# Kernel optimization log

Measured on AMD Instinct MI355X. Metric: run time of the kernel, lower is better.

Reference implementation:

```python
import jax, jax.numpy as jnp
from jax import lax
import numpy as np

B, L, D, H, SH = 4, 1024, 512, 8, 256
MLP_H = 4 * D
GAMMA, BETA = 0.1, 1.0
SIG_A, SIG_B = 1.0, 0.5
BIG = 1e9


def setup_inputs() -> dict:
    key = jax.random.key(0)
    ks = jax.random.split(key, 8)

    def lin(k, fin, fout):
        return jax.random.normal(k, (fin, fout), jnp.float32) * (1.0 / np.sqrt(fin))

    inp = {}
    inp["x"] = jax.random.normal(ks[0], (B, L, D), jnp.float32)
    inp["ln1_g"] = jnp.ones((D,), jnp.float32)
    inp["ln1_b"] = jnp.zeros((D,), jnp.float32)
    inp["ln2_g"] = jnp.ones((D,), jnp.float32)
    inp["ln2_b"] = jnp.zeros((D,), jnp.float32)
    inp["qkv_w"] = lin(ks[1], D, 3 * D)
    inp["qkv_b"] = jnp.zeros((3 * D,), jnp.float32)
    inp["proj_w"] = lin(ks[2], D, D)
    inp["proj_b"] = jnp.zeros((D,), jnp.float32)
    inp["fc1_w"] = lin(ks[3], D, MLP_H)
    inp["fc1_b"] = jnp.zeros((MLP_H,), jnp.float32)
    inp["fc2_w"] = lin(ks[4], MLP_H, D)
    inp["fc2_b"] = jnp.zeros((D,), jnp.float32)
    # 4 SigmaNets (norm1, attn, norm2, mlp) stacked on leading axis
    inp["sig_w1"] = jax.random.normal(ks[5], (4, D, SH), jnp.float32) * (1.0 / np.sqrt(D))
    inp["sig_b1"] = jnp.zeros((4, SH), jnp.float32)
    inp["sig_w2"] = jax.random.normal(ks[6], (4, SH, D), jnp.float32) * (1.0 / np.sqrt(SH))
    inp["sig_b2"] = jnp.zeros((4, D), jnp.float32)
    return inp


def layernorm(x, g, b, eps=1e-5):
    m = x.mean(-1, keepdims=True)
    v = ((x - m) ** 2).mean(-1, keepdims=True)
    return (x - m) / jnp.sqrt(v + eps) * g + b


def sigmanet(x, w1, b1, w2, b2):
    # (B,L,D) -> (B,L,1), sigma = a*sigmoid(mean(fc2(relu(fc1(x))))) + b
    h = jax.nn.relu(x @ w1 + b1)
    o = h @ w2 + b2
    m = o.mean(-1, keepdims=True)
    return SIG_A * jax.nn.sigmoid(m) + SIG_B


def attention(x, qkv_w, qkv_b, proj_w, proj_b):
    b_, l_, d_ = x.shape
    hd = d_ // H
    qkv = (x @ qkv_w + qkv_b).reshape(b_, l_, 3, H, hd)
    q, k, v = qkv[:, :, 0], qkv[:, :, 1], qkv[:, :, 2]  # (B,L,H,hd)
    scores = jnp.einsum("bqhd,bkhd->bhqk", q, k) * (hd ** -0.5)
    attn = jax.nn.softmax(scores, axis=-1)
    out = jnp.einsum("bhqk,bkhd->bqhd", attn, v).reshape(b_, l_, d_)
    return out @ proj_w + proj_b


def mlp(x, fc1_w, fc1_b, fc2_w, fc2_b):
    return jax.nn.gelu(x @ fc1_w + fc1_b, approximate=False) @ fc2_w + fc2_b


def soft_dtw(C, gamma):
    # soft-min DP over (B, N, N) cost matrix via anti-diagonal scan
    b_, n_, m_ = C.shape
    i_arr = jnp.arange(n_)

    def step(carry, k):
        d2, d1 = carry  # diagonals k-2, k-1; entry i holds R[i, (k-?)-i]
        j = k - i_arr
        valid = (j >= 0) & (j < m_)
        jc = jnp.clip(j, 0, m_ - 1)
        Cd = jnp.where(valid[None, :], C[:, i_arr, jc], BIG)
        pad = jnp.full((b_, 1), BIG, C.dtype)
        a = jnp.concatenate([pad, d2[:, :-1]], axis=1)  # R[i-1, j-1]
        a = a.at[:, 0].set(jnp.where(k == 0, 0.0, a[:, 0]))  # virtual R[-1,-1]=0
        bdiag = jnp.concatenate([pad, d1[:, :-1]], axis=1)  # R[i-1, j]
        c = d1  # R[i, j-1]
        smin = -gamma * jax.nn.logsumexp(-jnp.stack([a, bdiag, c], 0) / gamma, axis=0)
        new = jnp.where(valid[None, :], Cd + smin, BIG)
        return (d1, new), None

    init = (jnp.full((b_, n_), BIG, C.dtype), jnp.full((b_, n_), BIG, C.dtype))
    (_, last), _ = lax.scan(step, init, jnp.arange(n_ + m_ - 1))
    return last[:, n_ - 1]  # R[N-1, M-1]


def udtw(x, y, sx, sy):
    # pairwise squared distances without (B,L,L,D) intermediate
    x2 = jnp.sum(x * x, -1)  # (B,L)
    y2 = jnp.sum(y * y, -1)
    Dm = x2[:, :, None] + y2[:, None, :] - 2.0 * jnp.einsum("bnd,bmd->bnm", x, y)
    Dm = jnp.maximum(Dm, 0.0)
    Sig = sx ** 2 + jnp.swapaxes(sy, 1, 2) ** 2  # (B,L,L) sigma_i^2 + sigma_j^2
    d = soft_dtw(Dm / Sig, GAMMA)               # uncertainty-weighted distance path
    s = soft_dtw(BETA * jnp.log(Sig), GAMMA)    # sigma regularization path
    return d, s


def reference(x, ln1_g, ln1_b, ln2_g, ln2_b, qkv_w, qkv_b, proj_w, proj_b,
              fc1_w, fc1_b, fc2_w, fc2_b, sig_w1, sig_b1, sig_w2, sig_b2):
    orig = x
    attn_out = attention(layernorm(x, ln1_g, ln1_b), qkv_w, qkv_b, proj_w, proj_b)
    sigma_x = sigmanet(orig, sig_w1[0], sig_b1[0], sig_w2[0], sig_b2[0])
    sigma_attn = sigmanet(attn_out, sig_w1[1], sig_b1[1], sig_w2[1], sig_b2[1])
    d_a, s_a = udtw(orig, attn_out, sigma_x, sigma_attn)
    x = x + attn_out * sigma_attn  # merge_mode == 'mul'
    mlp_out = mlp(layernorm(x, ln2_g, ln2_b), fc1_w, fc1_b, fc2_w, fc2_b)
    sigma_x2 = sigmanet(orig, sig_w1[2], sig_b1[2], sig_w2[2], sig_b2[2])
    sigma_mlp = sigmanet(mlp_out, sig_w1[3], sig_b1[3], sig_w2[3], sig_b2[3])
    d_m, s_m = udtw(orig, mlp_out, sigma_x2, sigma_mlp)
    l_ = x.shape[1]
    aux_loss = (d_a.mean() + s_a.mean() + d_m.mean() + s_m.mean()) / (l_ * l_)
    x = x + mlp_out * sigma_mlp
    return x, aux_loss
```

## Files before the change

### kernel.cpp

```cpp
#include <hip/hip_runtime.h>
#include <math.h>

typedef unsigned short ushort;
typedef __attribute__((ext_vector_type(8))) short short8;
typedef __attribute__((ext_vector_type(4))) short short4v;
typedef __attribute__((ext_vector_type(4))) float f32x4;

#define DEVI static __device__ __forceinline__

constexpr int Bq = 4, Lq = 1024, Dq = 512, Hq = 8, SHq = 256;
constexpr int Mrows = Bq * Lq;
constexpr float BIGF = 1e9f;
constexpr int PSTR = 1048576 + 16;

DEVI float bf2f(ushort u) { union { unsigned u; float f; } v; v.u = ((unsigned)u) << 16; return v.f; }
DEVI float bf2f(short s) { return bf2f((ushort)s); }
DEVI ushort f2bf(float f) {
  union { float f; unsigned u; } v; v.f = f;
  unsigned r = v.u + 0x7fffu + ((v.u >> 16) & 1u);
  return (ushort)(r >> 16);
}
DEVI float wave_sum(float x) { for (int o = 1; o < 64; o <<= 1) x += __shfl_xor(x, o, 64); return x; }
DEVI float readin(const void* p, long i, int isf32) {
  return isf32 ? ((const float*)p)[i] : bf2f(((const ushort*)p)[i]);
}

__global__ void detect_kern(const unsigned* __restrict__ g, int* __restrict__ flag) {
  if (threadIdx.x == 0) flag[0] = (g[0] == 0x3F800000u) ? 1 : 0;
}

__global__ __launch_bounds__(256) void convx_kern(const void* __restrict__ src, ushort* __restrict__ dst,
                                                  long n, const int* __restrict__ flag) {
  const int f = *flag;
  for (long i = blockIdx.x * 256L + threadIdx.x; i < n; i += (long)gridDim.x * 256)
    dst[i] = f ? f2bf(((const float*)src)[i]) : ((const ushort*)src)[i];
}

__global__ __launch_bounds__(256) void conv9_kern(const void* p0, const void* p1, const void* p2,
                                                  const void* p3, const void* p4, const void* p5,
                                                  const void* p6, const void* p7, const void* p8,
                                                  ushort* __restrict__ dst, const int* __restrict__ flag) {
  const int off[10] = {0, 512, 1024, 1536, 2048, 3584, 4096, 6144, 6656, 7680};
  const void* ps[9] = {p0, p1, p2, p3, p4, p5, p6, p7, p8};
  const int b = blockIdx.x;
  const void* s = ps[b];
  const int n = off[b + 1] - off[b];
  const int f = *flag;
  for (int i = threadIdx.x; i < n; i += 256)
    dst[off[b] + i] = f ? f2bf(((const float*)s)[i]) : ((const ushort*)s)[i];
}

__global__ __launch_bounds__(256) void transpose_bf(const void* __restrict__ src,
                                                    ushort* __restrict__ dst, int R, int C,
                                                    const int* __restrict__ flag) {
  __shared__ ushort t[64][65];
  const int f = *flag;
  const int tx = threadIdx.x & 63, tg = threadIdx.x >> 6;
  const long base = (long)blockIdx.z * R * C;
  const int r0 = blockIdx.y * 64, c0 = blockIdx.x * 64;
#pragma unroll
  for (int i = 0; i < 16; ++i) {
    int y = tg * 16 + i;
    float v = readin(src, base + (long)(r0 + y) * C + c0 + tx, f);
    t[y][tx] = f2bf(v);
  }
  __syncthreads();
#pragma unroll
  for (int i = 0; i < 16; ++i) {
    int y = tg * 16 + i;
    dst[base + (long)(c0 + y) * R + r0 + tx] = t[tx][y];
  }
}

__global__ void w2bar_kern(const void* __restrict__ w2, float* __restrict__ w2bar,
                           const int* __restrict__ flag) {
  const int k = blockIdx.x, s = blockIdx.y, lane = threadIdx.x;
  const int f = *flag;
  float t = 0.f;
#pragma unroll
  for (int i = 0; i < 8; ++i) t += readin(w2, ((long)s * SHq + k) * Dq + lane * 8 + i, f);
  t = wave_sum(t);
  if (lane == 0) w2bar[s * SHq + k] = t * (1.f / Dq);
}
__global__ void b2bar_kern(const void* __restrict__ b2, float* __restrict__ b2bar,
                           const int* __restrict__ flag) {
  const int s = blockIdx.x, lane = threadIdx.x;
  const int f = *flag;
  float t = 0.f;
#pragma unroll
  for (int i = 0; i < 8; ++i) t += readin(b2, (long)s * Dq + lane * 8 + i, f);
  t = wave_sum(t);
  if (lane == 0) b2bar[s] = t * (1.f / Dq);
}

__global__ __launch_bounds__(256) void ln_kern(const ushort* __restrict__ x, const ushort* __restrict__ g,
                                               const ushort* __restrict__ b, ushort* __restrict__ out) {
  const int row = blockIdx.x * 4 + (threadIdx.x >> 6);
  const int lane = threadIdx.x & 63;
  short8 v = *(const short8*)(x + (long)row * Dq + lane * 8);
  float f[8]; float s = 0.f, s2 = 0.f;
#pragma unroll
  for (int i = 0; i < 8; ++i) { f[i] = bf2f(v[i]); s += f[i]; s2 += f[i] * f[i]; }
  s = wave_sum(s); s2 = wave_sum(s2);
  float mean = s * (1.f / Dq);
  float var = s2 * (1.f / Dq) - mean * mean;
  float rstd = rsqrtf(var + 1e-5f);
  short8 gv = *(const short8*)(g + lane * 8);
  short8 bv = *(const short8*)(b + lane * 8);
  short8 o;
#pragma unroll
  for (int i = 0; i < 8; ++i) o[i] = (short)f2bf((f[i] - mean) * rstd * bf2f(gv[i]) + bf2f(bv[i]));
  *(short8*)(out + (long)row * Dq + lane * 8) = o;
}

template<int EPI>
__global__ __launch_bounds__(256) void gemm_kern(
    const ushort* __restrict__ A, int lda, long sA,
    const ushort* __restrict__ Bt, int ldb, long sB,
    const ushort* __restrict__ bias,
    void* __restrict__ Cout, int ldc, long sC, int K,
    const float* __restrict__ vx2, const float* __restrict__ vy2,
    const float* __restrict__ vsx, const float* __restrict__ vsy) {
  constexpr int LDT = 40;
  __shared__ alignas(16) short As[128 * LDT];
  __shared__ alignas(16) short Bs[128 * LDT];
  const int tid = threadIdx.x, lane = tid & 63, wid = tid >> 6;
  const int wr = wid >> 1, wc = wid & 1;
  const int m0 = blockIdx.y * 128, n0 = blockIdx.x * 128;
  const int bz = blockIdx.z;
  const ushort* Ab = A + (long)bz * sA;
  const ushort* Bb = Bt + (long)bz * sB;
  const int sr = tid >> 2, sc = (tid & 3) * 8;
  const int lr = lane & 15, lk = (lane >> 4) * 8;
  f32x4 acc[4][4];
#pragma unroll
  for (int i = 0; i < 4; ++i)
#pragma unroll
    for (int j = 0; j < 4; ++j) acc[i][j] = f32x4{0.f, 0.f, 0.f, 0.f};

  for (int k0 = 0; k0 < K; k0 += 32) {
    short8 a0 = *(const short8*)(Ab + (long)(m0 + sr) * lda + k0 + sc);
    short8 a1 = *(const short8*)(Ab + (long)(m0 + sr + 64) * lda + k0 + sc);
    short8 b0 = *(const short8*)(Bb + (long)(n0 + sr) * ldb + k0 + sc);
    short8 b1 = *(const short8*)(Bb + (long)(n0 + sr + 64) * ldb + k0 + sc);
    __syncthreads();
    *(short8*)&As[sr * LDT + sc] = a0;
    *(short8*)&As[(sr + 64) * LDT + sc] = a1;
    *(short8*)&Bs[sr * LDT + sc] = b0;
    *(short8*)&Bs[(sr + 64) * LDT + sc] = b1;
    __syncthreads();
    short8 af[4], bg[4];
#pragma unroll
    for (int m = 0; m < 4; ++m) af[m] = *(const short8*)&As[(wr * 64 + m * 16 + lr) * LDT + lk];
#pragma unroll
    for (int n = 0; n < 4; ++n) bg[n] = *(const short8*)&Bs[(wc * 64 + n * 16 + lr) * LDT + lk];
#pragma unroll
    for (int m = 0; m < 4; ++m)
#pragma unroll
      for (int n = 0; n < 4; ++n)
        acc[m][n] = __builtin_amdgcn_mfma_f32_16x16x32_bf16(af[m], bg[n], acc[m][n], 0, 0, 0);
  }
  const int lq = (lane >> 4) * 4;
#pragma unroll
  for (int n = 0; n < 4; ++n) {
    const int col = n0 + wc * 64 + n * 16 + lr;
    float bia = 0.f, y2v = 0.f, syv = 0.f;
    if (EPI <= 2) { if (bias) bia = bf2f(bias[col]); }
    if (EPI == 3) { y2v = vy2[(long)bz * Lq + col]; float t = vsy[(long)bz * Lq + col]; syv = t * t; }
#pragma unroll
    for (int m = 0; m < 4; ++m) {
      f32x4 v = acc[m][n];
      if (EPI <= 2) {
#pragma unroll
        for (int q = 0; q < 4; ++q) {
          const int row = m0 + wr * 64 + m * 16 + lq + q;
          float c = v[q] + bia;
          if (EPI == 1) c = fmaxf(c, 0.f);
          if (EPI == 2) c = 0.5f * c * (1.f + erff(c * 0.70710678118654752f));
          ((ushort*)Cout)[(long)bz * sC + (long)row * ldc + col] = f2bf(c);
        }
      } else {
        const int row0 = m0 + wr * 64 + m * 16 + lq;
        f32x4 o;
#pragma unroll
        for (int q = 0; q < 4; ++q) {
          float x2v = vx2[(long)bz * Lq + row0 + q];
          float sxv = vsx[(long)bz * Lq + row0 + q];
          float dm = fmaxf(x2v + y2v - 2.f * v[q], 0.f);
          o[q] = dm / (sxv * sxv + syv);
        }
        *(f32x4*)((float*)Cout + (long)bz * sC + (long)col * 1024 + row0) = o;
      }
    }
  }
}

__global__ __launch_bounds__(256) void attn_kern(const ushort* __restrict__ qkv, ushort* __restrict__ octx) {
  const int qt = blockIdx.x, h = blockIdx.y, b = blockIdx.z;
  const int tid = threadIdx.x, lane = tid & 63, wid = tid >> 6;
  const int lr = lane & 15, lkg = lane >> 4;
  __shared__ alignas(16) short Ks[64 * 72];
  __shared__ alignas(16) short Vt[64 * 72];
  __shared__ alignas(16) short Ps[64 * 72];
  const long qrow0 = (long)b * Lq + qt * 64;
  short8 qf[2];
  {
    const ushort* qp = qkv + (qrow0 + wid * 16 + lr) * 1536 + h * 64;
    qf[0] = *(const short8*)(qp + lkg * 8);
    qf[1] = *(const short8*)(qp + 32 + lkg * 8);
  }
  f32x4 accO[4];
#pragma unroll
  for (int n = 0; n < 4; ++n) accO[n] = f32x4{0.f, 0.f, 0.f, 0.f};
  float mrun[4], lrun[4];
#pragma unroll
  for (int q = 0; q < 4; ++q) { mrun[q] = -1e30f; lrun[q] = 0.f; }

  for (int t = 0; t < 16; ++t) {
    __syncthreads();
#pragma unroll
    for (int i = 0; i < 2; ++i) {
      const int row = (tid >> 3) + i * 32;
      const int c8 = (tid & 7) * 8;
      const long gr = ((long)b * Lq + t * 64 + row) * 1536 + h * 64;
      short8 kv = *(const short8*)(qkv + gr + 512 + c8);
      *(short8*)&Ks[row * 72 + c8] = kv;
      short8 vv = *(const short8*)(qkv + gr + 1024 + c8);
#pragma unroll
      for (int j = 0; j < 8; ++j) Vt[(c8 + j) * 72 + row] = vv[j];
    }
    __syncthreads();
    f32x4 sf[4];
#pragma unroll
    for (int n = 0; n < 4; ++n) {
      sf[n] = f32x4{0.f, 0.f, 0.f, 0.f};
#pragma unroll
      for (int ks = 0; ks < 2; ++ks) {
        short8 bk = *(const short8*)&Ks[(n * 16 + lr) * 72 + ks * 32 + lkg * 8];
        sf[n] = __builtin_amdgcn_mfma_f32_16x16x32_bf16(qf[ks], bk, sf[n], 0, 0, 0);
      }
    }
#pragma unroll
    for (int n = 0; n < 4; ++n)
#pragma unroll
      for (int q = 0; q < 4; ++q) sf[n][q] *= 0.125f;
    float scl[4];
#pragma unroll
    for (int q = 0; q < 4; ++q) {
      float mx = fmaxf(fmaxf(sf[0][q], sf[1][q]), fmaxf(sf[2][q], sf[3][q]));
#pragma unroll
      for (int o = 1; o < 16; o <<= 1) mx = fmaxf(mx, __shfl_xor(mx, o, 64));
      float mnew = fmaxf(mrun[q], mx);
      scl[q] = __expf(mrun[q] - mnew);
      mrun[q] = mnew;
      float rs = 0.f;
#pragma unroll
      for (int n = 0; n < 4; ++n) { float pp = __expf(sf[n][q] - mnew); sf[n][q] = pp; rs += pp; }
#pragma unroll
      for (int o = 1; o < 16; o <<= 1) rs += __shfl_xor(rs, o, 64);
      lrun[q] = lrun[q] * scl[q] + rs;
    }
#pragma unroll
    for (int n = 0; n < 4; ++n)
#pragma unroll
      for (int q = 0; q < 4; ++q) accO[n][q] *= scl[q];
#pragma unroll
    for (int n = 0; n < 4; ++n)
#pragma unroll
      for (int q = 0; q < 4; ++q)
        Ps[(wid * 16 + lkg * 4 + q) * 72 + n * 16 + lr] = (short)f2bf(sf[n][q]);
    short8 pa[2];
    pa[0] = *(const short8*)&Ps[(wid * 16 + lr) * 72 + lkg * 8];
    pa[1] = *(const short8*)&Ps[(wid * 16 + lr) * 72 + 32 + lkg * 8];
#pragma unroll
    for (int n = 0; n < 4; ++n)
#pragma unroll
      for (int ks = 0; ks < 2; ++ks) {
        short8 bv = *(const short8*)&Vt[(n * 16 + lr) * 72 + ks * 32 + lkg * 8];
        accO[n] = __builtin_amdgcn_mfma_f32_16x16x32_bf16(pa[ks], bv, accO[n], 0, 0, 0);
      }
  }
#pragma unroll
  for (int n = 0; n < 4; ++n) {
    const int col = h * 64 + n * 16 + lr;
#pragma unroll
    for (int q = 0; q < 4; ++q) {
      const long row = qrow0 + wid * 16 + lkg * 4 + q;
      octx[row * 512 + col] = f2bf(accO[n][q] / fmaxf(lrun[q], 1e-30f));
    }
  }
}

__global__ __launch_bounds__(256) void rownorm2_kern(const ushort* __restrict__ x, float* __restrict__ out) {
  const int row = blockIdx.x * 4 + (threadIdx.x >> 6), lane = threadIdx.x & 63;
  short8 v = *(const short8*)(x + (long)row * Dq + lane * 8);
  float s = 0.f;
#pragma unroll
  for (int i = 0; i < 8; ++i) { float f = bf2f(v[i]); s += f * f; }
  s = wave_sum(s);
  if (lane == 0) out[row] = s;
}

__global__ __launch_bounds__(256) void sigma_reduce_kern(const ushort* __restrict__ h, const float* __restrict__ w2bar,
                                                         const float* __restrict__ b2bar, int set,
                                                         float* __restrict__ sigma) {
  const int row = blockIdx.x * 4 + (threadIdx.x >> 6), lane = threadIdx.x & 63;
  short4v hv = *(const short4v*)(h + (long)row * SHq + lane * 4);
  float s = 0.f;
#pragma unroll
  for (int i = 0; i < 4; ++i) s += bf2f(hv[i]) * w2bar[lane * 4 + i];
  s = wave_sum(s);
  if (lane == 0) {
    float m = s + b2bar[set];
    sigma[(long)set * Mrows + row] = 1.f / (1.f + __expf(-m)) + 0.5f;
  }
}

__global__ __launch_bounds__(256) void fuse1_kern(const ushort* __restrict__ x, const ushort* __restrict__ attn,
                                                  const float* __restrict__ sig, const ushort* __restrict__ g,
                                                  const ushort* __restrict__ bb, void* __restrict__ x1out,
                                                  ushort* __restrict__ xn2, const int* __restrict__ flag) {
  const int row = blockIdx.x * 4 + (threadIdx.x >> 6), lane = threadIdx.x & 63;
  const int isf32 = *flag;
  const float sg = sig[row];
  short8 xv = *(const short8*)(x + (long)row * Dq + lane * 8);
  short8 av = *(const short8*)(attn + (long)row * Dq + lane * 8);
  float f[8]; float s = 0.f, s2 = 0.f;
#pragma unroll
  for (int i = 0; i < 8; ++i) {
    f[i] = bf2f(xv[i]) + bf2f(av[i]) * sg;
    s += f[i]; s2 += f[i] * f[i];
  }
  if (isf32) {
    float* o32 = (float*)x1out + (long)row * Dq + lane * 8;
    *(f32x4*)o32 = f32x4{f[0], f[1], f[2], f[3]};
    *(f32x4*)(o32 + 4) = f32x4{f[4], f[5], f[6], f[7]};
  } else {
    short8 xo;
#pragma unroll
    for (int i = 0; i < 8; ++i) xo[i] = (short)f2bf(f[i]);
    *(short8*)((ushort*)x1out + (long)row * Dq + lane * 8) = xo;
  }
  s = wave_sum(s); s2 = wave_sum(s2);
  float mean = s * (1.f / Dq);
  float var = s2 * (1.f / Dq) - mean * mean;
  float rstd = rsqrtf(var + 1e-5f);
  short8 gv = *(const short8*)(g + lane * 8);
  short8 bv = *(const short8*)(bb + lane * 8);
  short8 o;
#pragma unroll
  for (int i = 0; i < 8; ++i) o[i] = (short)f2bf((f[i] - mean) * rstd * bf2f(gv[i]) + bf2f(bv[i]));
  *(short8*)(xn2 + (long)row * Dq + lane * 8) = o;
}

__global__ __launch_bounds__(256) void fuse2_kern(const ushort* __restrict__ mlp,
                                                  const float* __restrict__ sig, void* __restrict__ out,
                                                  const int* __restrict__ flag) {
  const int row = blockIdx.x * 4 + (threadIdx.x >> 6), lane = threadIdx.x & 63;
  const int isf32 = *flag;
  const float sg = sig[row];
  short8 mv = *(const short8*)(mlp + (long)row * Dq + lane * 8);
  if (isf32) {
    float* o32 = (float*)out + (long)row * Dq + lane * 8;
    f32x4 a = *(const f32x4*)o32;
    f32x4 b = *(const f32x4*)(o32 + 4);
#pragma unroll
    for (int i = 0; i < 4; ++i) a[i] += bf2f(mv[i]) * sg;
#pragma unroll
    for (int i = 0; i < 4; ++i) b[i] += bf2f(mv[4 + i]) * sg;
    *(f32x4*)o32 = a;
    *(f32x4*)(o32 + 4) = b;
  } else {
    ushort* o16 = (ushort*)out + (long)row * Dq + lane * 8;
    short8 xv = *(const short8*)o16;
    short8 o;
#pragma unroll
    for (int i = 0; i < 8; ++i) o[i] = (short)f2bf(bf2f(xv[i]) + bf2f(mv[i]) * sg);
    *(short8*)o16 = o;
  }
}

__global__ __launch_bounds__(128, 1) void dtw_kern(const float* __restrict__ Cta, const float* __restrict__ Ctm,
                                                   const float* __restrict__ sigma, float* __restrict__ res) {
  const int sid = blockIdx.x >> 2, b = blockIdx.x & 3;
  const int tid = threadIdx.x, lane = tid & 63, wid = tid >> 6;
  const bool isS = (sid & 1);
  __shared__ alignas(16) float smemf[18432];
  constexpr float LN2 = 0.69314718055994531f;

  float cur[16];
#pragma unroll
  for (int r = 0; r < 16; ++r) cur[r] = BIGF;
  float A = BIGF;
  float B = BIGF;
  float D = (lane == 0) ? 0.f : BIGF;

  if (!isS) {
    const float* Ct = ((sid == 0) ? Cta : Ctm) + (long)b * PSTR;

#define PRODUCE2(S0)                                                           \
    {                                                                          \
      f32x4 L[4][8];                                                           \
      _Pragma("unroll")                                                        \
      for (int j = 0; j < 4; ++j) {                                            \
        const int ss = (S0) + j;                                               \
        int cA = 2 * ss - 2 * lane;                                            \
        int cB = cA + 1;                                                       \
        cA = cA < 0 ? 0 : (cA > 1023 ? 1023 : cA);                             \
        cB = cB < 0 ? 0 : (cB > 1023 ? 1023 : cB);                             \
        const float* gA = Ct + (long)cA * 1024 + lane * 16;                    \
        const float* gB = Ct + (long)cB * 1024 + lane * 16;                    \
        _Pragma("unroll")                                                      \
        for (int q = 0; q < 4; ++q) { L[j][q] = *(const f32x4*)(gA + q * 4);   \
                                      L[j][4 + q] = *(const f32x4*)(gB + q * 4); } \
      }                                                                        \
      __builtin_amdgcn_sched_barrier(0);                                       \
      _Pragma("unroll")                                                        \
      for (int j = 0; j < 4; ++j) {                                            \
        float* lp = &smemf[(((S0) + j) & 7) * 2304 + lane * 36];               \
        _Pragma("unroll")                                                      \
        for (int q = 0; q < 4; ++q) { *(f32x4*)(lp + q * 4) = L[j][q];         \
                                      *(f32x4*)(lp + 16 + q * 4) = L[j][4 + q]; } \
      }                                                                        \
    }

#define DSTEP2(S, CHK)                                                         \
    {                                                                          \
      const float* lp = &smemf[((S) & 7) * 2304 + lane * 36];                  \
      f32x4 ra[4], rb[4];                                                      \
      _Pragma("unroll")                                                        \
      for (int q = 0; q < 4; ++q) { ra[q] = *(const f32x4*)(lp + q * 4);       \
                                    rb[q] = *(const f32x4*)(lp + 16 + q * 4); } \
      const int c1 = 2 * (S) - 2 * lane;                                       \
      const bool v1 = (unsigned)c1 < 1024u;                                    \
      const bool v2 = (unsigned)(c1 + 1) < 1024u;                              \
      float above = A, diag = D;                                               \
      _Pragma("unroll")                                                        \
      for (int i = 0; i < 16; ++i) {                                           \
        float tmp = cur[i];                                                    \
        float v = ra[i >> 2][i & 3] + fminf(fminf(above, tmp), diag);          \
        cur[i] = (CHK) ? (v1 ? v : tmp) : v;                                   \
        diag = tmp; above = v;                                                 \
      }                                                                        \
      float bot1 = cur[15];                                                    \
      above = B; diag = A;                                                     \
      _Pragma("unroll")                                                        \
      for (int i = 0; i < 16; ++i) {                                           \
        float tmp = cur[i];                                                    \
        float v = rb[i >> 2][i & 3] + fminf(fminf(above, tmp), diag);          \
        cur[i] = (CHK) ? (v2 ? v : tmp) : v;                                   \
        diag = tmp; above = v;                                                 \
      }                                                                        \
      float bot2 = cur[15];                                                    \
      D = B;                                                                   \
      float sA = __shfl_up(bot1, 1, 64);                                       \
      float sB = __shfl_up(bot2, 1, 64);                                       \
      A = (lane == 0) ? BIGF : sA;                                             \
      B = (lane == 0) ? BIGF : sB;                                             \
    }

    if (wid == 1) PRODUCE2(0)
    __syncthreads();
#pragma clang loop unroll(disable)
    for (int p = 0; p < 16; ++p) {
      if (wid == 1) { PRODUCE2(4 * p + 4) }
      else { const int s0 = 4 * p; DSTEP2(s0, 1) DSTEP2(s0 + 1, 1) DSTEP2(s0 + 2, 1) DSTEP2(s0 + 3, 1) }
      __syncthreads();
    }
#pragma clang loop unroll(disable)
    for (int p = 16; p < 128; ++p) {
      if (wid == 1) { PRODUCE2(4 * p + 4) }
      else { const int s0 = 4 * p; DSTEP2(s0, 0) DSTEP2(s0 + 1, 0) DSTEP2(s0 + 2, 0) DSTEP2(s0 + 3, 0) }
      __syncthreads();
    }
#pragma clang loop unroll(disable)
    for (int p = 128; p < 144; ++p) {
      if (wid == 1) { if (p < 143) PRODUCE2(4 * p + 4) }
      else { const int s0 = 4 * p; DSTEP2(s0, 1) DSTEP2(s0 + 1, 1) DSTEP2(s0 + 2, 1) DSTEP2(s0 + 3, 1) }
      __syncthreads();
    }
#undef PRODUCE2
#undef DSTEP2
    if (wid == 0 && lane == 63) res[blockIdx.x] = cur[15];
  } else {
    const int sxset = (sid == 1) ? 0 : 2;
    const float* sxv = sigma + (long)sxset * Mrows + b * Lq;
    const float* syv = sigma + (long)(sxset + 1) * Mrows + b * Lq;
    for (int i = tid; i < Lq; i += 128) { float v = syv[i]; smemf[i] = v * v; }
    __syncthreads();
    if (wid == 1) return;
    float sx2[16];
#pragma unroll
    for (int r = 0; r < 16; ++r) { float t = sxv[16 * lane + r]; sx2[r] = t * t; }
    int ia = -2 * lane; ia = ia < 0 ? 0 : ia;
    int ib = 1 - 2 * lane; ib = ib < 0 ? 0 : ib;
    float syA = smemf[ia], syB = smemf[ib];

#define SSTEP2(S, CHK)                                                         \
    {                                                                          \
      int na = 2 * ((S) + 1) - 2 * lane; na = na < 0 ? 0 : (na > 1023 ? 1023 : na); \
      int nb = na + 1; nb = nb > 1023 ? 1023 : nb;                             \
      float syA_n = smemf[na], syB_n = smemf[nb];                              \
      const int c1 = 2 * (S) - 2 * lane;                                       \
      const bool v1 = (unsigned)c1 < 1024u;                                    \
      const bool v2 = (unsigned)(c1 + 1) < 1024u;                              \
      float above = A, diag = D;                                               \
      _Pragma("unroll")                                                        \
      for (int i = 0; i < 16; ++i) {                                           \
        float tmp = cur[i];                                                    \
        float cv = LN2 * __builtin_amdgcn_logf(sx2[i] + syA);                  \
        float v = cv + fminf(fminf(above, tmp), diag);                         \
        cur[i] = (CHK) ? (v1 ? v : tmp) : v;                                   \
        diag = tmp; above = v;                                                 \
      }                                                                        \
      float bot1 = cur[15];                                                    \
      above = B; diag = A;                                                     \
      _Pragma("unroll")                                                        \
      for (int i = 0; i < 16; ++i) {                                           \
        float tmp = cur[i];                                                    \
        float cv = LN2 * __builtin_amdgcn_logf(sx2[i] + syB);                  \
        float v = cv + fminf(fminf(above, tmp), diag);                         \
        cur[i] = (CHK) ? (v2 ? v : tmp) : v;                                   \
        diag = tmp; above = v;                                                 \
      }                                                                        \
      float bot2 = cur[15];                                                    \
      D = B; syA = syA_n; syB = syB_n;                                         \
      float sA = __shfl_up(bot1, 1, 64);                                       \
      float sB = __shfl_up(bot2, 1, 64);                                       \
      A = (lane == 0) ? BIGF : sA;                                             \
      B = (lane == 0) ? BIGF : sB;                                             \
    }

#pragma clang loop unroll(disable)
    for (int s = 0; s < 63; ++s) SSTEP2(s, 1)
#pragma clang loop unroll(disable)
    for (int s = 63; s < 512; ++s) SSTEP2(s, 0)
#pragma clang loop unroll(disable)
    for (int s = 512; s < 576; ++s) SSTEP2(s, 1)
#undef SSTEP2
    if (lane == 63) res[blockIdx.x] = cur[15];
  }
}

__global__ void aux_kern(const float* __restrict__ res, void* __restrict__ out,
                         const int* __restrict__ flag) {
  if (threadIdx.x == 0) {
    float s = 0.f;
    for (int i = 0; i < 16; ++i) s += res[i];
    float v = s * (0.25f / (1024.f * 1024.f));
    if (*flag) ((float*)out)[(size_t)Mrows * 512] = v;
    else       ((ushort*)out)[(size_t)Mrows * 512] = f2bf(v);
  }
}

extern "C" void kernel_launch(void* const* d_in, const int* in_sizes, int n_in,
                              void* d_out, int out_size, void* d_ws, size_t ws_size,
                              hipStream_t stream) {
  const void* x_raw   = d_in[0];
  const void* ln1_g   = d_in[1];
  const void* ln1_b   = d_in[2];
  const void* ln2_g   = d_in[3];
  const void* ln2_b   = d_in[4];
  const void* qkv_w   = d_in[5];
  const void* qkv_b   = d_in[6];
  const void* proj_w  = d_in[7];
  const void* proj_b  = d_in[8];
  const void* fc1_w   = d_in[9];
  const void* fc1_b   = d_in[10];
  const void* fc2_w   = d_in[11];
  const void* fc2_b   = d_in[12];
  const void* sig_w1  = d_in[13];
  const void* sig_b1  = d_in[14];
  const void* sig_w2  = d_in[15];
  const void* sig_b2  = d_in[16];

  char* p = (char*)d_ws;
  auto alloc = [&](size_t n) { char* r = p; p += (n + 255) & ~(size_t)255; return r; };
  const size_t REGION = (size_t)4 * PSTR * 4;
  int*    flag    = (int*)alloc(256);
  ushort* csmall  = (ushort*)alloc(7680 * 2);
  ushort* x_bf    = (ushort*)alloc((size_t)Mrows * 512 * 2);
  ushort* wt_qkv  = (ushort*)alloc((size_t)1536 * 512 * 2);
  ushort* wt_proj = (ushort*)alloc((size_t)512 * 512 * 2);
  ushort* wt_fc1  = (ushort*)alloc((size_t)2048 * 512 * 2);
  ushort* wt_fc2  = (ushort*)alloc((size_t)512 * 2048 * 2);
  ushort* wt_sig1 = (ushort*)alloc((size_t)4 * 256 * 512 * 2);
  float*  w2bar   = (float*)alloc(4 * 256 * 4);
  float*  b2bar   = (float*)alloc(4 * 4);
  ushort* xnorm   = (ushort*)alloc((size_t)Mrows * 512 * 2);
  char* region1 = alloc(REGION);
  ushort* qkvb     = (ushort*)region1;
  ushort* attn_ctx = (ushort*)(region1 + (size_t)Mrows * 1536 * 2);
  float*  Cta      = (float*)region1;
  ushort* abuf   = (ushort*)alloc((size_t)Mrows * 512 * 2);
  ushort* hsig   = (ushort*)alloc((size_t)Mrows * 256 * 2);
  float*  sigma  = (float*)alloc((size_t)4 * Mrows * 4);
  float*  x2n    = (float*)alloc(Mrows * 4);
  float*  y2a    = (float*)alloc(Mrows * 4);
  float*  y2m    = (float*)alloc(Mrows * 4);
  char* region2 = alloc(REGION);
  ushort* h1  = (ushort*)region2;
  float*  Ctm = (float*)region2;
  float*  dres = (float*)alloc(64 * 4);

  const ushort* c_ln1g = csmall + 0;
  const ushort* c_ln1b = csmall + 512;
  const ushort* c_ln2g = csmall + 1024;
  const ushort* c_ln2b = csmall + 1536;
  const ushort* c_qkvb = csmall + 2048;
  const ushort* c_projb = csmall + 3584;
  const ushort* c_fc1b = csmall + 4096;
  const ushort* c_fc2b = csmall + 6144;
  const ushort* c_sigb1 = csmall + 6656;

  detect_kern<<<1, 64, 0, stream>>>((const unsigned*)ln1_g, flag);
  conv9_kern<<<9, 256, 0, stream>>>(ln1_g, ln1_b, ln2_g, ln2_b, qkv_b, proj_b, fc1_b, fc2_b, sig_b1,
                                    csmall, flag);
  convx_kern<<<2048, 256, 0, stream>>>(x_raw, x_bf, (long)Mrows * 512, flag);

  transpose_bf<<<dim3(24, 8, 1), 256, 0, stream>>>(qkv_w, wt_qkv, 512, 1536, flag);
  transpose_bf<<<dim3(8, 8, 1), 256, 0, stream>>>(proj_w, wt_proj, 512, 512, flag);
  transpose_bf<<<dim3(32, 8, 1), 256, 0, stream>>>(fc1_w, wt_fc1, 512, 2048, flag);
  transpose_bf<<<dim3(8, 32, 1), 256, 0, stream>>>(fc2_w, wt_fc2, 2048, 512, flag);
  transpose_bf<<<dim3(4, 8, 4), 256, 0, stream>>>(sig_w1, wt_sig1, 512, 256, flag);
  w2bar_kern<<<dim3(256, 4), 64, 0, stream>>>(sig_w2, w2bar, flag);
  b2bar_kern<<<4, 64, 0, stream>>>(sig_b2, b2bar, flag);

  ln_kern<<<Mrows / 4, 256, 0, stream>>>(x_bf, c_ln1g, c_ln1b, xnorm);
  gemm_kern<0><<<dim3(12, 32, 1), 256, 0, stream>>>(xnorm, 512, 0, wt_qkv, 512, 0, c_qkvb,
                                                    qkvb, 1536, 0, 512, nullptr, nullptr, nullptr, nullptr);
  attn_kern<<<dim3(16, 8, 4), 256, 0, stream>>>(qkvb, attn_ctx);
  gemm_kern<0><<<dim3(4, 32, 1), 256, 0, stream>>>(attn_ctx, 512, 0, wt_proj, 512, 0, c_projb,
                                                   abuf, 512, 0, 512, nullptr, nullptr, nullptr, nullptr);
  gemm_kern<1><<<dim3(2, 32, 1), 256, 0, stream>>>(x_bf, 512, 0, wt_sig1, 512, 0, c_sigb1,
                                                   hsig, 256, 0, 512, nullptr, nullptr, nullptr, nullptr);
  sigma_reduce_kern<<<Mrows / 4, 256, 0, stream>>>(hsig, w2bar, b2bar, 0, sigma);
  gemm_kern<1><<<dim3(2, 32, 1), 256, 0, stream>>>(abuf, 512, 0, wt_sig1 + 1 * 256 * 512, 512, 0, c_sigb1 + 256,
                                                   hsig, 256, 0, 512, nullptr, nullptr, nullptr, nullptr);
  sigma_reduce_kern<<<Mrows / 4, 256, 0, stream>>>(hsig, w2bar + 256, b2bar, 1, sigma);
  rownorm2_kern<<<Mrows / 4, 256, 0, stream>>>(x_bf, x2n);
  rownorm2_kern<<<Mrows / 4, 256, 0, stream>>>(abuf, y2a);
  gemm_kern<3><<<dim3(8, 8, 4), 256, 0, stream>>>(x_bf, 512, (long)1024 * 512, abuf, 512, (long)1024 * 512, nullptr,
                                                  Cta, 1024, (long)PSTR, 512, x2n, y2a, sigma, sigma + Mrows);
  fuse1_kern<<<Mrows / 4, 256, 0, stream>>>(x_bf, abuf, sigma + Mrows, c_ln2g, c_ln2b, d_out, xnorm, flag);
  gemm_kern<2><<<dim3(16, 32, 1), 256, 0, stream>>>(xnorm, 512, 0, wt_fc1, 512, 0, c_fc1b,
                                                    h1, 2048, 0, 512, nullptr, nullptr, nullptr, nullptr);
  gemm_kern<0><<<dim3(4, 32, 1), 256, 0, stream>>>(h1, 2048, 0, wt_fc2, 2048, 0, c_fc2b,
                                                   abuf, 512, 0, 2048, nullptr, nullptr, nullptr, nullptr);
  gemm_kern<1><<<dim3(2, 32, 1), 256, 0, stream>>>(x_bf, 512, 0, wt_sig1 + 2 * 256 * 512, 512, 0, c_sigb1 + 512,
                                                   hsig, 256, 0, 512, nullptr, nullptr, nullptr, nullptr);
  sigma_reduce_kern<<<Mrows / 4, 256, 0, stream>>>(hsig, w2bar + 512, b2bar, 2, sigma);
  gemm_kern<1><<<dim3(2, 32, 1), 256, 0, stream>>>(abuf, 512, 0, wt_sig1 + 3 * 256 * 512, 512, 0, c_sigb1 + 768,
                                                   hsig, 256, 0, 512, nullptr, nullptr, nullptr, nullptr);
  sigma_reduce_kern<<<Mrows / 4, 256, 0, stream>>>(hsig, w2bar + 768, b2bar, 3, sigma);
  rownorm2_kern<<<Mrows / 4, 256, 0, stream>>>(abuf, y2m);
  gemm_kern<3><<<dim3(8, 8, 4), 256, 0, stream>>>(x_bf, 512, (long)1024 * 512, abuf, 512, (long)1024 * 512, nullptr,
                                                  Ctm, 1024, (long)PSTR, 512, x2n, y2m,
                                                  sigma + 2 * Mrows, sigma + 3 * Mrows);
  fuse2_kern<<<Mrows / 4, 256, 0, stream>>>(abuf, sigma + 3 * Mrows, d_out, flag);
  dtw_kern<<<16, 128, 0, stream>>>(Cta, Ctm, sigma, dres);
  aux_kern<<<1, 64, 0, stream>>>(dres, d_out, flag);
}
```

Baseline: 549.2 us.

## Merge prep kernels into one launch, fuse row-norm into LN, pipeline DTW loads

Folds the conversion, transpose and w2bar/b2bar prep kernels into a single block-indexed prep kernel, which cuts about nine launches. The x row sum of squares now comes out of the first layernorm, so one rownorm pass is dropped. The soft-DTW consumer loop now double-buffers its shared-memory loads, fetching step s+1 while the chain for step s runs, to hide LDS latency. The cost is higher register pressure in the DTW loop and a larger branchy prep kernel.

```diff
diff --git a/kernel.cpp b/kernel.cpp
--- a/kernel.cpp
+++ b/kernel.cpp
@@ -29,35 +29,23 @@
   if (threadIdx.x == 0) flag[0] = (g[0] == 0x3F800000u) ? 1 : 0;
 }
 
-__global__ __launch_bounds__(256) void convx_kern(const void* __restrict__ src, ushort* __restrict__ dst,
-                                                  long n, const int* __restrict__ flag) {
-  const int f = *flag;
-  for (long i = blockIdx.x * 256L + threadIdx.x; i < n; i += (long)gridDim.x * 256)
-    dst[i] = f ? f2bf(((const float*)src)[i]) : ((const ushort*)src)[i];
-}
-
-__global__ __launch_bounds__(256) void conv9_kern(const void* p0, const void* p1, const void* p2,
-                                                  const void* p3, const void* p4, const void* p5,
-                                                  const void* p6, const void* p7, const void* p8,
-                                                  ushort* __restrict__ dst, const int* __restrict__ flag) {
-  const int off[10] = {0, 512, 1024, 1536, 2048, 3584, 4096, 6144, 6656, 7680};
-  const void* ps[9] = {p0, p1, p2, p3, p4, p5, p6, p7, p8};
-  const int b = blockIdx.x;
-  const void* s = ps[b];
-  const int n = off[b + 1] - off[b];
-  const int f = *flag;
-  for (int i = threadIdx.x; i < n; i += 256)
-    dst[off[b] + i] = f ? f2bf(((const float*)s)[i]) : ((const ushort*)s)[i];
-}
-
-__global__ __launch_bounds__(256) void transpose_bf(const void* __restrict__ src,
-                                                    ushort* __restrict__ dst, int R, int C,
-                                                    const int* __restrict__ flag) {
-  __shared__ ushort t[64][65];
-  const int f = *flag;
+struct PrepArgs {
+  const void *ln1_g, *ln1_b, *ln2_g, *ln2_b, *qkv_b, *proj_b, *fc1_b, *fc2_b, *sig_b1;
+  ushort* csmall;
+  const void* x_raw; ushort* x_bf;
+  const void *qkv_w, *proj_w, *fc1_w, *fc2_w, *sig_w1;
+  ushort *wt_qkv, *wt_proj, *wt_fc1, *wt_fc2, *wt_sig1;
+  const void *sig_w2;
+  const void *sig_b2;
+  float *w2bar, *b2bar;
+  const int* flag;
+};
+
+DEVI void do_transpose(const void* src, ushort* dst, int R, int C, int bx, int by, int bz, int f,
+                       ushort (*t)[65]) {
   const int tx = threadIdx.x & 63, tg = threadIdx.x >> 6;
-  const long base = (long)blockIdx.z * R * C;
-  const int r0 = blockIdx.y * 64, c0 = blockIdx.x * 64;
+  const long base = (long)bz * R * C;
+  const int r0 = by * 64, c0 = bx * 64;
 #pragma unroll
   for (int i = 0; i < 16; ++i) {
     int y = tg * 16 + i;
@@ -72,29 +60,59 @@
   }
 }
 
-__global__ void w2bar_kern(const void* __restrict__ w2, float* __restrict__ w2bar,
-                           const int* __restrict__ flag) {
-  const int k = blockIdx.x, s = blockIdx.y, lane = threadIdx.x;
-  const int f = *flag;
-  float t = 0.f;
-#pragma unroll
-  for (int i = 0; i < 8; ++i) t += readin(w2, ((long)s * SHq + k) * Dq + lane * 8 + i, f);
-  t = wave_sum(t);
-  if (lane == 0) w2bar[s * SHq + k] = t * (1.f / Dq);
-}
-__global__ void b2bar_kern(const void* __restrict__ b2, float* __restrict__ b2bar,
-                           const int* __restrict__ flag) {
-  const int s = blockIdx.x, lane = threadIdx.x;
-  const int f = *flag;
-  float t = 0.f;
-#pragma unroll
-  for (int i = 0; i < 8; ++i) t += readin(b2, (long)s * Dq + lane * 8 + i, f);
-  t = wave_sum(t);
-  if (lane == 0) b2bar[s] = t * (1.f / Dq);
+__global__ __launch_bounds__(256) void prep_kern(PrepArgs a) {
+  __shared__ ushort t[64][65];
+  const int bid = blockIdx.x, tid = threadIdx.x;
+  const int f = *a.flag;
+  if (bid < 9) {
+    const int off[10] = {0, 512, 1024, 1536, 2048, 3584, 4096, 6144, 6656, 7680};
+    const void* ps[9] = {a.ln1_g, a.ln1_b, a.ln2_g, a.ln2_b, a.qkv_b, a.proj_b, a.fc1_b, a.fc2_b, a.sig_b1};
+    const void* s = ps[bid];
+    const int n = off[bid + 1] - off[bid];
+    for (int i = tid; i < n; i += 256)
+      a.csmall[off[bid] + i] = f ? f2bf(((const float*)s)[i]) : ((const ushort*)s)[i];
+  } else if (bid < 2057) {
+    const long c0 = (long)(bid - 9) * 1024;
+    for (int i = tid; i < 1024; i += 256)
+      a.x_bf[c0 + i] = f ? f2bf(((const float*)a.x_raw)[c0 + i]) : ((const ushort*)a.x_raw)[c0 + i];
+  } else if (bid < 2313) {
+    const int wid = tid >> 6, lane = tid & 63;
+    const int p = (bid - 2057) * 4 + wid;
+    const int k = p & 255, s = p >> 8;
+    float acc = 0.f;
+#pragma unroll
+    for (int i = 0; i < 8; ++i) acc += readin(a.sig_w2, ((long)s * SHq + k) * Dq + lane * 8 + i, f);
+    acc = wave_sum(acc);
+    if (lane == 0) a.w2bar[s * SHq + k] = acc * (1.f / Dq);
+  } else if (bid < 2314) {
+    const int wid = tid >> 6, lane = tid & 63;
+    float acc = 0.f;
+#pragma unroll
+    for (int i = 0; i < 8; ++i) acc += readin(a.sig_b2, (long)wid * Dq + lane * 8 + i, f);
+    acc = wave_sum(acc);
+    if (lane == 0) a.b2bar[wid] = acc * (1.f / Dq);
+  } else if (bid < 2506) {
+    const int lb = bid - 2314;
+    do_transpose(a.qkv_w, a.wt_qkv, 512, 1536, lb % 24, lb / 24, 0, f, t);
+  } else if (bid < 2570) {
+    const int lb = bid - 2506;
+    do_transpose(a.proj_w, a.wt_proj, 512, 512, lb % 8, lb / 8, 0, f, t);
+  } else if (bid < 2826) {
+    const int lb = bid - 2570;
+    do_transpose(a.fc1_w, a.wt_fc1, 512, 2048, lb % 32, lb / 32, 0, f, t);
+  } else if (bid < 3082) {
+    const int lb = bid - 2826;
+    do_transpose(a.fc2_w, a.wt_fc2, 2048, 512, lb % 8, lb / 8, 0, f, t);
+  } else {
+    const int lb = bid - 3082;
+    const int z = lb / 32, rem = lb % 32;
+    do_transpose(a.sig_w1, a.wt_sig1, 512, 256, rem % 4, rem / 4, z, f, t);
+  }
 }
 
 __global__ __launch_bounds__(256) void ln_kern(const ushort* __restrict__ x, const ushort* __restrict__ g,
-                                               const ushort* __restrict__ b, ushort* __restrict__ out) {
+                                               const ushort* __restrict__ b, ushort* __restrict__ out,
+                                               float* __restrict__ x2out) {
   const int row = blockIdx.x * 4 + (threadIdx.x >> 6);
   const int lane = threadIdx.x & 63;
   short8 v = *(const short8*)(x + (long)row * Dq + lane * 8);
@@ -102,6 +120,7 @@
 #pragma unroll
   for (int i = 0; i < 8; ++i) { f[i] = bf2f(v[i]); s += f[i]; s2 += f[i] * f[i]; }
   s = wave_sum(s); s2 = wave_sum(s2);
+  if (lane == 0) x2out[row] = s2;
   float mean = s * (1.f / Dq);
   float var = s2 * (1.f / Dq) - mean * mean;
   float rstd = rsqrtf(var + 1e-5f);
@@ -424,13 +443,16 @@
       }                                                                        \
     }
 
-#define DSTEP2(S, CHK)                                                         \
+#define LOADR(RA, RB, S)                                                       \
     {                                                                          \
       const float* lp = &smemf[((S) & 7) * 2304 + lane * 36];                  \
-      f32x4 ra[4], rb[4];                                                      \
       _Pragma("unroll")                                                        \
-      for (int q = 0; q < 4; ++q) { ra[q] = *(const f32x4*)(lp + q * 4);       \
-                                    rb[q] = *(const f32x4*)(lp + 16 + q * 4); } \
+      for (int q = 0; q < 4; ++q) { RA[q] = *(const f32x4*)(lp + q * 4);       \
+                                    RB[q] = *(const f32x4*)(lp + 16 + q * 4); } \
+    }
+
+#define DCHAIN2(S, RA, RB, CHK)                                                \
+    {                                                                          \
       const int c1 = 2 * (S) - 2 * lane;                                       \
       const bool v1 = (unsigned)c1 < 1024u;                                    \
       const bool v2 = (unsigned)(c1 + 1) < 1024u;                              \
@@ -438,7 +460,7 @@
       _Pragma("unroll")                                                        \
       for (int i = 0; i < 16; ++i) {                                           \
         float tmp = cur[i];                                                    \
-        float v = ra[i >> 2][i & 3] + fminf(fminf(above, tmp), diag);          \
+        float v = RA[i >> 2][i & 3] + fminf(fminf(above, tmp), diag);          \
         cur[i] = (CHK) ? (v1 ? v : tmp) : v;                                   \
         diag = tmp; above = v;                                                 \
       }                                                                        \
@@ -447,7 +469,7 @@
       _Pragma("unroll")                                                        \
       for (int i = 0; i < 16; ++i) {                                           \
         float tmp = cur[i];                                                    \
-        float v = rb[i >> 2][i & 3] + fminf(fminf(above, tmp), diag);          \
+        float v = RB[i >> 2][i & 3] + fminf(fminf(above, tmp), diag);          \
         cur[i] = (CHK) ? (v2 ? v : tmp) : v;                                   \
         diag = tmp; above = v;                                                 \
       }                                                                        \
@@ -459,28 +481,40 @@
       B = (lane == 0) ? BIGF : sB;                                             \
     }
 
+#define DPHASE4(S0, CHK)                                                       \
+    {                                                                          \
+      f32x4 pa[4], pb[4], qa[4], qb[4];                                        \
+      LOADR(pa, pb, (S0) + 0)                                                  \
+      LOADR(qa, qb, (S0) + 1)                                                  \
+      DCHAIN2((S0) + 0, pa, pb, CHK)                                           \
+      LOADR(pa, pb, (S0) + 2)                                                  \
+      DCHAIN2((S0) + 1, qa, qb, CHK)                                           \
+      LOADR(qa, qb, (S0) + 3)                                                  \
+      DCHAIN2((S0) + 2, pa, pb, CHK)                                           \
+      DCHAIN2((S0) + 3, qa, qb, CHK)                                           \
+    }
+
     if (wid == 1) PRODUCE2(0)
     __syncthreads();
 #pragma clang loop unroll(disable)
     for (int p = 0; p < 16; ++p) {
-      if (wid == 1) { PRODUCE2(4 * p + 4) }
-      else { const int s0 = 4 * p; DSTEP2(s0, 1) DSTEP2(s0 + 1, 1) DSTEP2(s0 + 2, 1) DSTEP2(s0 + 3, 1) }
+      if (wid == 1) { PRODUCE2(4 * p + 4) } else { DPHASE4(4 * p, 1) }
       __syncthreads();
     }
 #pragma clang loop unroll(disable)
     for (int p = 16; p < 128; ++p) {
-      if (wid == 1) { PRODUCE2(4 * p + 4) }
-      else { const int s0 = 4 * p; DSTEP2(s0, 0) DSTEP2(s0 + 1, 0) DSTEP2(s0 + 2, 0) DSTEP2(s0 + 3, 0) }
+      if (wid == 1) { PRODUCE2(4 * p + 4) } else { DPHASE4(4 * p, 0) }
       __syncthreads();
     }
 #pragma clang loop unroll(disable)
     for (int p = 128; p < 144; ++p) {
-      if (wid == 1) { if (p < 143) PRODUCE2(4 * p + 4) }
-      else { const int s0 = 4 * p; DSTEP2(s0, 1) DSTEP2(s0 + 1, 1) DSTEP2(s0 + 2, 1) DSTEP2(s0 + 3, 1) }
+      if (wid == 1) { if (p < 143) PRODUCE2(4 * p + 4) } else { DPHASE4(4 * p, 1) }
       __syncthreads();
     }
 #undef PRODUCE2
-#undef DSTEP2
+#undef LOADR
+#undef DCHAIN2
+#undef DPHASE4
     if (wid == 0 && lane == 63) res[blockIdx.x] = cur[15];
   } else {
     const int sxset = (sid == 1) ? 0 : 2;
@@ -614,19 +648,16 @@
   const ushort* c_sigb1 = csmall + 6656;
 
   detect_kern<<<1, 64, 0, stream>>>((const unsigned*)ln1_g, flag);
-  conv9_kern<<<9, 256, 0, stream>>>(ln1_g, ln1_b, ln2_g, ln2_b, qkv_b, proj_b, fc1_b, fc2_b, sig_b1,
-                                    csmall, flag);
-  convx_kern<<<2048, 256, 0, stream>>>(x_raw, x_bf, (long)Mrows * 512, flag);
-
-  transpose_bf<<<dim3(24, 8, 1), 256, 0, stream>>>(qkv_w, wt_qkv, 512, 1536, flag);
-  transpose_bf<<<dim3(8, 8, 1), 256, 0, stream>>>(proj_w, wt_proj, 512, 512, flag);
-  transpose_bf<<<dim3(32, 8, 1), 256, 0, stream>>>(fc1_w, wt_fc1, 512, 2048, flag);
-  transpose_bf<<<dim3(8, 32, 1), 256, 0, stream>>>(fc2_w, wt_fc2, 2048, 512, flag);
-  transpose_bf<<<dim3(4, 8, 4), 256, 0, stream>>>(sig_w1, wt_sig1, 512, 256, flag);
-  w2bar_kern<<<dim3(256, 4), 64, 0, stream>>>(sig_w2, w2bar, flag);
-  b2bar_kern<<<4, 64, 0, stream>>>(sig_b2, b2bar, flag);
-
-  ln_kern<<<Mrows / 4, 256, 0, stream>>>(x_bf, c_ln1g, c_ln1b, xnorm);
+  PrepArgs pa;
+  pa.ln1_g = ln1_g; pa.ln1_b = ln1_b; pa.ln2_g = ln2_g; pa.ln2_b = ln2_b;
+  pa.qkv_b = qkv_b; pa.proj_b = proj_b; pa.fc1_b = fc1_b; pa.fc2_b = fc2_b; pa.sig_b1 = sig_b1;
+  pa.csmall = csmall; pa.x_raw = x_raw; pa.x_bf = x_bf;
+  pa.qkv_w = qkv_w; pa.proj_w = proj_w; pa.fc1_w = fc1_w; pa.fc2_w = fc2_w; pa.sig_w1 = sig_w1;
+  pa.wt_qkv = wt_qkv; pa.wt_proj = wt_proj; pa.wt_fc1 = wt_fc1; pa.wt_fc2 = wt_fc2; pa.wt_sig1 = wt_sig1;
+  pa.sig_w2 = sig_w2; pa.sig_b2 = sig_b2; pa.w2bar = w2bar; pa.b2bar = b2bar; pa.flag = flag;
+  prep_kern<<<3210, 256, 0, stream>>>(pa);
+
+  ln_kern<<<Mrows / 4, 256, 0, stream>>>(x_bf, c_ln1g, c_ln1b, xnorm, x2n);
   gemm_kern<0><<<dim3(12, 32, 1), 256, 0, stream>>>(xnorm, 512, 0, wt_qkv, 512, 0, c_qkvb,
                                                     qkvb, 1536, 0, 512, nullptr, nullptr, nullptr, nullptr);
   attn_kern<<<dim3(16, 8, 4), 256, 0, stream>>>(qkvb, attn_ctx);
@@ -638,7 +669,6 @@
   gemm_kern<1><<<dim3(2, 32, 1), 256, 0, stream>>>(abuf, 512, 0, wt_sig1 + 1 * 256 * 512, 512, 0, c_sigb1 + 256,
                                                    hsig, 256, 0, 512, nullptr, nullptr, nullptr, nullptr);
   sigma_reduce_kern<<<Mrows / 4, 256, 0, stream>>>(hsig, w2bar + 256, b2bar, 1, sigma);
-  rownorm2_kern<<<Mrows / 4, 256, 0, stream>>>(x_bf, x2n);
   rownorm2_kern<<<Mrows / 4, 256, 0, stream>>>(abuf, y2a);
   gemm_kern<3><<<dim3(8, 8, 4), 256, 0, stream>>>(x_bf, 512, (long)1024 * 512, abuf, 512, (long)1024 * 512, nullptr,
                                                   Cta, 1024, (long)PSTR, 512, x2n, y2a, sigma, sigma + Mrows);
```

Measured after the change: 511.9 us. -6.8%, faster.
